# Performance work log

Measured on AMD Instinct MI355X. Metric: run time of the kernel, lower is better.

## Reference

```python
import jax, jax.numpy as jnp
import numpy as np

H, C, PQ, PV = 12, 16, 4, 8  # heads, scalar head dim, query points, value points
EPS = 1e-8


def setup_inputs() -> dict:
    key = jax.random.key(0)
    ks = jax.random.split(key, 16)
    B, N, S, Z = 2, 512, 384, 128
    def w(k, fan_in, shape):
        return jax.random.normal(k, shape, jnp.float32) / np.sqrt(fan_in)
    return {
        's': jax.random.normal(ks[0], (B, N, S), jnp.float32),
        'z': jax.random.normal(ks[1], (B, N, N, Z), jnp.float32),
        'R': jax.random.normal(ks[2], (B, N, 3, 3), jnp.float32),
        't': jax.random.normal(ks[3], (B, N, 3), jnp.float32),
        'Wq': w(ks[4], S, (S, H * C)),
        'Wk': w(ks[5], S, (S, H * C)),
        'Wv': w(ks[6], S, (S, H * C)),
        'Wqp': w(ks[7], S, (S, H * PQ * 3)),
        'Wkp': w(ks[8], S, (S, H * PQ * 3)),
        'Wvp': w(ks[9], S, (S, H * PV * 3)),
        'Wb': w(ks[10], Z, (Z, H)),
        'head_weights': jax.random.normal(ks[11], (H,), jnp.float32) * 0.1,
        'Wout': w(ks[12], H * (C + 4 * PV + Z), (H * (C + 4 * PV + Z), S)),
    }


def reference(s, z, R, t, Wq, Wk, Wv, Wqp, Wkp, Wvp, Wb, head_weights, Wout):
    B, N, _ = s.shape
    Zc = z.shape[-1]
    # scalar q/k/v: [B,N,H,C]
    q = (s @ Wq).reshape(B, N, H, C)
    k = (s @ Wk).reshape(B, N, H, C)
    v = (s @ Wv).reshape(B, N, H, C)
    # point q/k/v in local frames, then map to global: x_g = R x + t
    def to_global(Wp, P):
        p = (s @ Wp).reshape(B, N, H, P, 3)
        return jnp.einsum('bnxy,bnhpy->bnhpx', R, p) + t[:, :, None, None, :]
    qp = to_global(Wqp, PQ)   # [B,N,H,PQ,3]
    kp = to_global(Wkp, PQ)
    vp = to_global(Wvp, PV)   # [B,N,H,PV,3]
    # pair bias [B,H,N,N]
    b = jnp.einsum('bijz,zh->bhij', z, Wb)
    # scalar attention logits
    scal = jnp.einsum('bihc,bjhc->bhij', q, k) / np.sqrt(C)
    # squared point distances via expansion (avoid [B,N,N,H,PQ,3] tensor)
    qq = jnp.sum(qp * qp, axis=(-1, -2))                    # [B,N,H]
    kk = jnp.sum(kp * kp, axis=(-1, -2))                    # [B,N,H]
    qk = jnp.einsum('bihpx,bjhpx->bhij', qp, kp)
    dist2 = qq.transpose(0, 2, 1)[:, :, :, None] + kk.transpose(0, 2, 1)[:, :, None, :] - 2.0 * qk
    gamma = jax.nn.softplus(head_weights)                   # [H]
    wC = np.sqrt(2.0 / (9.0 * PQ))
    wL = np.sqrt(1.0 / 3.0)
    logits = wL * (scal + b) - (wL * wC / 2.0) * gamma[None, :, None, None] * dist2
    a = jax.nn.softmax(logits, axis=-1)                     # [B,H,N,N]
    # scalar output
    o = jnp.einsum('bhij,bjhc->bihc', a, v).reshape(B, N, H * C)
    # point output: aggregate in global frame, then back to local: R^T (x - t)
    opt_g = jnp.einsum('bhij,bjhpx->bihpx', a, vp)
    d = opt_g - t[:, :, None, None, :]
    opt = jnp.einsum('bnyx,bnhpy->bnhpx', R, d)             # R^T d
    opt_norm = jnp.sqrt(jnp.sum(opt * opt, axis=-1) + EPS)  # [B,N,H,PV]
    # pair output
    opair = jnp.einsum('bhij,bijz->bihz', a, z).reshape(B, N, H * Zc)
    cat = jnp.concatenate([o, opt.reshape(B, N, H * PV * 3),
                           opt_norm.reshape(B, N, H * PV), opair], axis=-1)
    return cat @ Wout
```

## Files before the change

kernel.cpp:

```cpp
#include <hip/hip_runtime.h>
#include <math.h>

#define BB 2
#define NN 512
#define SDIM 384
#define ZDIM 128
#define HH 12
#define CDIM 16
#define PQ 4
#define PV 8
#define BN (BB*NN)
#define CATD 2112

#define WL  0.57735026918962576f
#define LAM 0.06804138174397717f

#define OFF_Q    0
#define OFF_QP   196608
#define OFF_QQ   344064
#define OFF_KT4  356352
#define OFF_KPT4 552960
#define OFF_KKT  700416
#define OFF_V    712704
#define OFF_VP   909312
#define OFF_BIAS 1204224
#define OFF_CAT  7495680

__device__ __forceinline__ float dot4(float4 a, float4 b) {
    return a.x*b.x + a.y*b.y + a.z*b.z + a.w*b.w;
}
__device__ __forceinline__ void fma4(float4& a, float s, float4 b) {
    a.x += s*b.x; a.y += s*b.y; a.z += s*b.z; a.w += s*b.w;
}
__device__ __forceinline__ void add4(float4& a, float4 b) {
    a.x += b.x; a.y += b.y; a.z += b.z; a.w += b.w;
}
__device__ __forceinline__ void mul4(float4& a, float s) {
    a.x *= s; a.y *= s; a.z *= s; a.w *= s;
}

__global__ __launch_bounds__(256) void k_proj(
    const float* __restrict__ s, const float* __restrict__ Rg, const float* __restrict__ tg,
    const float* __restrict__ Wq, const float* __restrict__ Wk, const float* __restrict__ Wv,
    const float* __restrict__ Wqp, const float* __restrict__ Wkp, const float* __restrict__ Wvp,
    float* __restrict__ ws)
{
    __shared__ float4 pL4[2][144];
    __shared__ float  sqL[2][96];
    __shared__ float  Rt[2][12];
    const int t = threadIdx.x;
    const int n0 = blockIdx.x * 2;
    const int b  = n0 >> 9;
    const int nloc = n0 & 511;

    if (t < 24) {
        int rr = t / 12, c = t % 12;
        Rt[rr][c] = (c < 9) ? Rg[(n0+rr)*9 + c] : tg[(n0+rr)*3 + (c-9)];
    }
    const float* s0 = s + (size_t)n0*SDIM;
    const float* s1 = s0 + SDIM;
    __syncthreads();

    float4* Q4g  = (float4*)(ws + OFF_Q);
    float4* V4g  = (float4*)(ws + OFF_V);
    float4* KT4g = (float4*)(ws + OFF_KT4);

    for (int it = 0; it < 2; ++it) {
        int g = t + it*256;
        if (g >= 288) break;
        const float4* W4; int wc4, ld4, dst;
        if (g < 48)       { W4 = (const float4*)Wq;  wc4 = g;     ld4 = 48; dst = 0; }
        else if (g < 96)  { W4 = (const float4*)Wk;  wc4 = g-48;  ld4 = 48; dst = 1; }
        else if (g < 144) { W4 = (const float4*)Wv;  wc4 = g-96;  ld4 = 48; dst = 2; }
        else if (g < 180) { W4 = (const float4*)Wqp; wc4 = g-144; ld4 = 36; dst = 3; }
        else if (g < 216) { W4 = (const float4*)Wkp; wc4 = g-180; ld4 = 36; dst = 4; }
        else              { W4 = (const float4*)Wvp; wc4 = g-216; ld4 = 72; dst = 5; }
        float4 acc0 = {0,0,0,0}, acc1 = {0,0,0,0};
        #pragma unroll 4
        for (int r = 0; r < SDIM; ++r) {
            float4 wv = W4[r*ld4 + wc4];
            float f0 = s0[r], f1 = s1[r];
            fma4(acc0, f0, wv);
            fma4(acc1, f1, wv);
        }
        if (dst == 0) {
            Q4g[(size_t)n0*48 + wc4] = acc0;
            Q4g[(size_t)(n0+1)*48 + wc4] = acc1;
        } else if (dst == 1) {
            size_t base = ((size_t)(b*48 + wc4))*512 + nloc;
            KT4g[base] = acc0; KT4g[base+1] = acc1;
        } else if (dst == 2) {
            V4g[(size_t)n0*48 + wc4] = acc0;
            V4g[(size_t)(n0+1)*48 + wc4] = acc1;
        } else if (dst == 3) {
            pL4[0][wc4] = acc0; pL4[1][wc4] = acc1;
        } else if (dst == 4) {
            pL4[0][36+wc4] = acc0; pL4[1][36+wc4] = acc1;
        } else {
            pL4[0][72+wc4] = acc0; pL4[1][72+wc4] = acc1;
        }
    }
    __syncthreads();

    for (int task = t; task < 384; task += 256) {
        int rr = task / 192, pt = task % 192;
        const float* pl = (const float*)pL4[rr];
        int off = (pt < 48) ? pt*3 : (pt < 96 ? 144 + (pt-48)*3 : 288 + (pt-96)*3);
        float p0 = pl[off], p1 = pl[off+1], p2 = pl[off+2];
        const float* R = Rt[rr];
        float g0 = R[0]*p0 + R[1]*p1 + R[2]*p2 + R[9];
        float g1 = R[3]*p0 + R[4]*p1 + R[5]*p2 + R[10];
        float g2 = R[6]*p0 + R[7]*p1 + R[8]*p2 + R[11];
        int bn = n0 + rr, n = bn & 511;
        if (pt < 48) {
            int o = pt*3;
            float* d = ws + OFF_QP + (size_t)bn*144 + o;
            d[0] = g0; d[1] = g1; d[2] = g2;
            sqL[rr][pt] = g0*g0 + g1*g1 + g2*g2;
        } else if (pt < 96) {
            int pc = (pt-48)*3;
            float gg[3] = {g0,g1,g2};
            #pragma unroll
            for (int x = 0; x < 3; ++x) {
                int pcx = pc + x;
                ws[OFF_KPT4 + (((size_t)(b*36 + (pcx>>2)))*512 + n)*4 + (pcx&3)] = gg[x];
            }
            sqL[rr][pt] = g0*g0 + g1*g1 + g2*g2;
        } else {
            int o = (pt-96)*3;
            float* d = ws + OFF_VP + (size_t)bn*288 + o;
            d[0] = g0; d[1] = g1; d[2] = g2;
        }
    }
    __syncthreads();

    if (t < 48) {
        int rr = t / 24, u = t % 24;
        int bn = n0 + rr, n = bn & 511;
        if (u < 12) {
            float sm = sqL[rr][u*4] + sqL[rr][u*4+1] + sqL[rr][u*4+2] + sqL[rr][u*4+3];
            ws[OFF_QQ + (size_t)bn*12 + u] = sm;
        } else {
            int h = u - 12;
            float sm = sqL[rr][48+h*4] + sqL[rr][48+h*4+1] + sqL[rr][48+h*4+2] + sqL[rr][48+h*4+3];
            ws[OFF_KKT + ((size_t)(b*12 + h))*512 + n] = sm;
        }
    }
}

__global__ __launch_bounds__(256) void k_bias(
    const float* __restrict__ z, const float* __restrict__ Wb, float* __restrict__ ws)
{
    __shared__ __align__(16) float4 zsh[64*33];
    const int t = threadIdx.x;
    const int blk = blockIdx.x;
    const int bi = blk >> 3;
    const int j0 = (blk & 7) * 64;
    const float4* zg = (const float4*)z + ((size_t)bi*512 + j0)*32;
    #pragma unroll
    for (int k = 0; k < 8; ++k) {
        const int i = t + 256*k;
        zsh[(i>>5)*33 + (i&31)] = zg[i];
    }
    __syncthreads();

    const int j  = t >> 2;
    const int hg = t & 3;
    float a0 = 0.f, a1 = 0.f, a2 = 0.f;
    const float4* row = &zsh[j*33];
    #pragma unroll 8
    for (int c4 = 0; c4 < 32; ++c4) {
        const float4 zq = row[c4];
        const float* wb = Wb + c4*48;
        #pragma unroll
        for (int e = 0; e < 4; ++e) {
            const float zv = ((const float*)&zq)[e];
            const float* w = wb + e*12;
            a0 += zv * w[hg];
            a1 += zv * w[hg+4];
            a2 += zv * w[hg+8];
        }
    }
    float* BI = ws + OFF_BIAS + (size_t)bi*HH*512 + j0 + j;
    BI[(hg  )*512] = a0;
    BI[(hg+4)*512] = a1;
    BI[(hg+8)*512] = a2;
}

__global__ __launch_bounds__(512, 2) void k_attn(
    const float* __restrict__ z, const float* __restrict__ Rg, const float* __restrict__ tg,
    const float* __restrict__ hw, float* __restrict__ ws)
{
    __shared__ __align__(16) float aL[HH*516];
    __shared__ float4 optgS4[72];
    __shared__ float RiL[9], tiL[3], sInv[12];

    const int t = threadIdx.x;
    const int d = blockIdx.x;
    const int xcd = d & 7, slot = d >> 3;
    const int bi = (xcd < 4) ? (xcd*128 + slot) : (512 + (xcd-4)*128 + slot);
    const int b = bi >> 9;

    if (t < 9)             RiL[t]   = Rg[bi*9 + t];
    if (t >= 9 && t < 12)  tiL[t-9] = tg[bi*3 + (t-9)];

    float gam[HH];
    #pragma unroll
    for (int h = 0; h < HH; ++h) {
        float x = hw[h];
        gam[h] = (x > 20.f) ? x : log1pf(__expf(x));
    }

    {
        const int j = t;
        const float4* Q4u  = (const float4*)(ws + OFF_Q  + (size_t)bi*192);
        const float4* QP4u = (const float4*)(ws + OFF_QP + (size_t)bi*144);
        const float*  QQu  = ws + OFF_QQ + (size_t)bi*12;
        const float4* KT4  = (const float4*)(ws + OFF_KT4)  + (size_t)b*48*512;
        const float4* KPT4 = (const float4*)(ws + OFF_KPT4) + (size_t)b*36*512;
        const float*  KKT  = ws + OFF_KKT  + (size_t)b*12*512;
        const float*  BI   = ws + OFF_BIAS + (size_t)bi*HH*512;
        for (int h = 0; h < HH; ++h) {
            float scal = 0.f, qk = 0.f;
            #pragma unroll
            for (int cg = 0; cg < 4; ++cg)
                scal += dot4(Q4u[h*4+cg], KT4[(h*4+cg)*512 + j]);
            #pragma unroll
            for (int pg = 0; pg < 3; ++pg)
                qk += dot4(QP4u[h*3+pg], KPT4[(h*3+pg)*512 + j]);
            float dist2 = QQu[h] + KKT[h*512 + j] - 2.f*qk;
            aL[h*516 + j] = WL*(scal*0.25f + BI[h*512 + j]) - LAM*gam[h]*dist2;
        }
    }
    __syncthreads();

    {
        const int w = t >> 6, lane = t & 63;
        for (int h = w; h < HH; h += 8) {
            float* row = aL + h*516;
            float m = -1e30f;
            #pragma unroll
            for (int k = 0; k < 8; ++k) m = fmaxf(m, row[lane + 64*k]);
            #pragma unroll
            for (int off = 32; off > 0; off >>= 1) m = fmaxf(m, __shfl_xor(m, off));
            float ssum = 0.f;
            #pragma unroll
            for (int k = 0; k < 8; ++k) {
                float e = __expf(row[lane + 64*k] - m);
                row[lane + 64*k] = e;
                ssum += e;
            }
            #pragma unroll
            for (int off = 32; off > 0; off >>= 1) ssum += __shfl_xor(ssum, off);
            if (lane == 0) sInv[h] = 1.f / ssum;
        }
    }
    __syncthreads();

    float4 acc0 = {0,0,0,0}, acc1 = {0,0,0,0}, acc2 = {0,0,0,0};
    int rid = -1, seg = 0;

#define FMA8(ZB, AP0, AP1, AP2, JT) do { \
    float4 av0 = *(const float4*)((AP0) + (JT)); \
    float4 av1 = *(const float4*)((AP1) + (JT)); \
    float4 av2 = *(const float4*)((AP2) + (JT)); \
    float4 aw0 = *(const float4*)((AP0) + (JT) + 4); \
    float4 aw1 = *(const float4*)((AP1) + (JT) + 4); \
    float4 aw2 = *(const float4*)((AP2) + (JT) + 4); \
    fma4(acc0, av0.x, ZB[0]); fma4(acc1, av1.x, ZB[0]); fma4(acc2, av2.x, ZB[0]); \
    fma4(acc0, av0.y, ZB[1]); fma4(acc1, av1.y, ZB[1]); fma4(acc2, av2.y, ZB[1]); \
    fma4(acc0, av0.z, ZB[2]); fma4(acc1, av1.z, ZB[2]); fma4(acc2, av2.z, ZB[2]); \
    fma4(acc0, av0.w, ZB[3]); fma4(acc1, av1.w, ZB[3]); fma4(acc2, av2.w, ZB[3]); \
    fma4(acc0, aw0.x, ZB[4]); fma4(acc1, aw1.x, ZB[4]); fma4(acc2, aw2.x, ZB[4]); \
    fma4(acc0, aw0.y, ZB[5]); fma4(acc1, aw1.y, ZB[5]); fma4(acc2, aw2.y, ZB[5]); \
    fma4(acc0, aw0.z, ZB[6]); fma4(acc1, aw1.z, ZB[6]); fma4(acc2, aw2.z, ZB[6]); \
    fma4(acc0, aw0.w, ZB[7]); fma4(acc1, aw1.w, ZB[7]); fma4(acc2, aw2.w, ZB[7]); \
} while (0)

    if (t < 384) {
        seg = t >> 7;
        rid = t & 127;
        const int hg = rid >> 5, zc4 = rid & 31;
        const int j0 = seg*176;
        const int ngrp = (seg == 2) ? 20 : 22;
        const float4* Zp = (const float4*)z + (size_t)bi*512*32 + zc4;
        const float* a0p = aL + hg*516;
        const float* a1p = aL + (hg+4)*516;
        const float* a2p = aL + (hg+8)*516;
        float4 zA[8], zB[8];
        #pragma unroll
        for (int e = 0; e < 8; ++e) zA[e] = Zp[(size_t)(j0+e)*32];
        for (int p = 0; p < ngrp; p += 2) {
            const int jt = j0 + p*8;
            #pragma unroll
            for (int e = 0; e < 8; ++e) zB[e] = Zp[(size_t)(jt+8+e)*32];
            FMA8(zA, a0p, a1p, a2p, jt);
            if (p + 2 < ngrp) {
                #pragma unroll
                for (int e = 0; e < 8; ++e) zA[e] = Zp[(size_t)(jt+16+e)*32];
            }
            FMA8(zB, a0p, a1p, a2p, jt + 8);
        }
    } else if (t < 504) {
        const int v = t - 384;
        seg = v / 40;
        const int w = v % 40;
        rid = 128 + w;
        const int j0 = seg*176, j1 = (seg == 2) ? 512 : j0 + 176;
        const float4* P; int S, D, O, hg;
        if (w < 16) {
            hg = w >> 2; S = 48; D = 16; O = hg*4 + (w & 3);
            P = (const float4*)(ws + OFF_V) + (size_t)b*512*48;
        } else {
            const int v2 = w - 16;
            hg = v2 / 6; S = 72; D = 24; O = hg*6 + v2 % 6;
            P = (const float4*)(ws + OFF_VP) + (size_t)b*512*72;
        }
        const float* a0p = aL + hg*516;
        const float* a1p = aL + (hg+4)*516;
        const float* a2p = aL + (hg+8)*516;
        #pragma unroll 2
        for (int jt = j0; jt < j1; jt += 4) {
            float4 av0 = *(const float4*)(a0p + jt);
            float4 av1 = *(const float4*)(a1p + jt);
            float4 av2 = *(const float4*)(a2p + jt);
            #pragma unroll
            for (int e = 0; e < 4; ++e) {
                const size_t base = (size_t)(jt+e)*S + O;
                fma4(acc0, ((const float*)&av0)[e], P[base]);
                fma4(acc1, ((const float*)&av1)[e], P[base + D]);
                fma4(acc2, ((const float*)&av2)[e], P[base + 2*D]);
            }
        }
    }
    __syncthreads();
    float4* sc4 = (float4*)aL;
    if (rid >= 0) {
        const int si = (seg*168 + rid)*3;
        sc4[si] = acc0; sc4[si+1] = acc1; sc4[si+2] = acc2;
    }
    __syncthreads();

    if (t < 168) {
        float4 r0 = {0,0,0,0}, r1 = {0,0,0,0}, r2 = {0,0,0,0};
        #pragma unroll
        for (int ss = 0; ss < 3; ++ss) {
            const int si = (ss*168 + t)*3;
            add4(r0, sc4[si]); add4(r1, sc4[si+1]); add4(r2, sc4[si+2]);
        }
        int typ, hg;
        if (t < 128)      { typ = 0; hg = t >> 5; }
        else if (t < 144) { typ = 1; hg = (t-128) >> 2; }
        else              { typ = 2; hg = (t-144) / 6; }
        mul4(r0, sInv[hg]); mul4(r1, sInv[hg+4]); mul4(r2, sInv[hg+8]);
        float4* cat4 = (float4*)(ws + OFF_CAT);
        const size_t cb = (size_t)bi * 528;
        if (typ == 0) {
            const int zc4 = t & 31;
            cat4[cb + 144 + (hg  )*32 + zc4] = r0;
            cat4[cb + 144 + (hg+4)*32 + zc4] = r1;
            cat4[cb + 144 + (hg+8)*32 + zc4] = r2;
        } else if (typ == 1) {
            const int c4 = (t-128) & 3;
            cat4[cb + (hg  )*4 + c4] = r0;
            cat4[cb + (hg+4)*4 + c4] = r1;
            cat4[cb + (hg+8)*4 + c4] = r2;
        } else {
            const int po = (t-144) % 6;
            optgS4[(hg  )*6 + po] = r0;
            optgS4[(hg+4)*6 + po] = r1;
            optgS4[(hg+8)*6 + po] = r2;
        }
    }
    __syncthreads();

    if (t < 96) {
        const float* og = (const float*)optgS4;
        int h = t >> 3, p = t & 7;
        int o = h*24 + p*3;
        float d0 = og[o]   - tiL[0];
        float d1 = og[o+1] - tiL[1];
        float d2 = og[o+2] - tiL[2];
        float ox = RiL[0]*d0 + RiL[3]*d1 + RiL[6]*d2;
        float oy = RiL[1]*d0 + RiL[4]*d1 + RiL[7]*d2;
        float oz = RiL[2]*d0 + RiL[5]*d1 + RiL[8]*d2;
        float* cat = ws + OFF_CAT + (size_t)bi*CATD;
        cat[192 + o]     = ox;
        cat[192 + o + 1] = oy;
        cat[192 + o + 2] = oz;
        cat[480 + h*8 + p] = sqrtf(ox*ox + oy*oy + oz*oz + 1e-8f);
    }
}

__global__ __launch_bounds__(384) void k_out(
    const float* __restrict__ Wout, const float* __restrict__ ws, float* __restrict__ out)
{
    const int t = threadIdx.x;
    const int row0 = blockIdx.x * 4;
    const float* c0 = ws + OFF_CAT + (size_t)(row0+0)*CATD;
    const float* c1 = c0 + CATD;
    const float* c2 = c1 + CATD;
    const float* c3 = c2 + CATD;
    float a0 = 0.f, a1 = 0.f, a2 = 0.f, a3 = 0.f;
    #pragma unroll 8
    for (int r = 0; r < CATD; ++r) {
        float w = Wout[(size_t)r*384 + t];
        a0 += c0[r]*w; a1 += c1[r]*w; a2 += c2[r]*w; a3 += c3[r]*w;
    }
    out[(size_t)(row0+0)*384 + t] = a0;
    out[(size_t)(row0+1)*384 + t] = a1;
    out[(size_t)(row0+2)*384 + t] = a2;
    out[(size_t)(row0+3)*384 + t] = a3;
}

extern "C" void kernel_launch(void* const* d_in, const int* in_sizes, int n_in,
                              void* d_out, int out_size, void* d_ws, size_t ws_size,
                              hipStream_t stream)
{
    const float* s    = (const float*)d_in[0];
    const float* z    = (const float*)d_in[1];
    const float* R    = (const float*)d_in[2];
    const float* tt   = (const float*)d_in[3];
    const float* Wq   = (const float*)d_in[4];
    const float* Wk   = (const float*)d_in[5];
    const float* Wv   = (const float*)d_in[6];
    const float* Wqp  = (const float*)d_in[7];
    const float* Wkp  = (const float*)d_in[8];
    const float* Wvp  = (const float*)d_in[9];
    const float* Wb   = (const float*)d_in[10];
    const float* hw   = (const float*)d_in[11];
    const float* Wout = (const float*)d_in[12];
    float* ws  = (float*)d_ws;
    float* out = (float*)d_out;

    hipLaunchKernelGGL(k_proj, dim3(BN/2),     dim3(256), 0, stream,
                       s, R, tt, Wq, Wk, Wv, Wqp, Wkp, Wvp, ws);
    hipLaunchKernelGGL(k_bias, dim3(BN*NN/64), dim3(256), 0, stream, z, Wb, ws);
    hipLaunchKernelGGL(k_attn, dim3(BN),       dim3(512), 0, stream, z, R, tt, hw, ws);
    hipLaunchKernelGGL(k_out,  dim3(BN/4),     dim3(384), 0, stream, Wout, ws, out);
}
```

Before: 803.3 us.

## Fuse pair-bias projection into attention kernel, drop separate bias pass

Removes the standalone k_bias kernel and computes the z·Wb pair bias per (i,j) directly inside k_attn, with each thread reading its own z row from global memory. This avoids writing and re-reading the bias buffer and saves one launch. z still has to be read again later for the pair-output aggregation. The in-kernel reads are strided per thread (each thread reads a 512-byte row), and the 12 extra accumulators add register pressure under launch_bounds(512,2).

```diff
diff --git a/kernel.cpp b/kernel.cpp
--- a/kernel.cpp
+++ b/kernel.cpp
@@ -23,7 +23,6 @@
 #define OFF_KKT  700416
 #define OFF_V    712704
 #define OFF_VP   909312
-#define OFF_BIAS 1204224
 #define OFF_CAT  7495680
 
 __device__ __forceinline__ float dot4(float4 a, float4 b) {
@@ -148,48 +147,9 @@
     }
 }
 
-__global__ __launch_bounds__(256) void k_bias(
-    const float* __restrict__ z, const float* __restrict__ Wb, float* __restrict__ ws)
-{
-    __shared__ __align__(16) float4 zsh[64*33];
-    const int t = threadIdx.x;
-    const int blk = blockIdx.x;
-    const int bi = blk >> 3;
-    const int j0 = (blk & 7) * 64;
-    const float4* zg = (const float4*)z + ((size_t)bi*512 + j0)*32;
-    #pragma unroll
-    for (int k = 0; k < 8; ++k) {
-        const int i = t + 256*k;
-        zsh[(i>>5)*33 + (i&31)] = zg[i];
-    }
-    __syncthreads();
-
-    const int j  = t >> 2;
-    const int hg = t & 3;
-    float a0 = 0.f, a1 = 0.f, a2 = 0.f;
-    const float4* row = &zsh[j*33];
-    #pragma unroll 8
-    for (int c4 = 0; c4 < 32; ++c4) {
-        const float4 zq = row[c4];
-        const float* wb = Wb + c4*48;
-        #pragma unroll
-        for (int e = 0; e < 4; ++e) {
-            const float zv = ((const float*)&zq)[e];
-            const float* w = wb + e*12;
-            a0 += zv * w[hg];
-            a1 += zv * w[hg+4];
-            a2 += zv * w[hg+8];
-        }
-    }
-    float* BI = ws + OFF_BIAS + (size_t)bi*HH*512 + j0 + j;
-    BI[(hg  )*512] = a0;
-    BI[(hg+4)*512] = a1;
-    BI[(hg+8)*512] = a2;
-}
-
 __global__ __launch_bounds__(512, 2) void k_attn(
     const float* __restrict__ z, const float* __restrict__ Rg, const float* __restrict__ tg,
-    const float* __restrict__ hw, float* __restrict__ ws)
+    const float* __restrict__ hw, const float* __restrict__ Wb, float* __restrict__ ws)
 {
     __shared__ __align__(16) float aL[HH*516];
     __shared__ float4 optgS4[72];
@@ -213,13 +173,28 @@
 
     {
         const int j = t;
+        float pb[HH];
+        #pragma unroll
+        for (int h = 0; h < HH; ++h) pb[h] = 0.f;
+        const float4* zrow4 = (const float4*)z + ((size_t)bi*512 + j)*32;
+        #pragma unroll 4
+        for (int c4 = 0; c4 < 32; ++c4) {
+            const float4 zq = zrow4[c4];
+            const float* wb = Wb + c4*48;
+            #pragma unroll
+            for (int e = 0; e < 4; ++e) {
+                const float zv = ((const float*)&zq)[e];
+                const float* w = wb + e*12;
+                #pragma unroll
+                for (int h = 0; h < HH; ++h) pb[h] += zv * w[h];
+            }
+        }
         const float4* Q4u  = (const float4*)(ws + OFF_Q  + (size_t)bi*192);
         const float4* QP4u = (const float4*)(ws + OFF_QP + (size_t)bi*144);
         const float*  QQu  = ws + OFF_QQ + (size_t)bi*12;
         const float4* KT4  = (const float4*)(ws + OFF_KT4)  + (size_t)b*48*512;
         const float4* KPT4 = (const float4*)(ws + OFF_KPT4) + (size_t)b*36*512;
         const float*  KKT  = ws + OFF_KKT  + (size_t)b*12*512;
-        const float*  BI   = ws + OFF_BIAS + (size_t)bi*HH*512;
         for (int h = 0; h < HH; ++h) {
             float scal = 0.f, qk = 0.f;
             #pragma unroll
@@ -229,7 +204,7 @@
             for (int pg = 0; pg < 3; ++pg)
                 qk += dot4(QP4u[h*3+pg], KPT4[(h*3+pg)*512 + j]);
             float dist2 = QQu[h] + KKT[h*512 + j] - 2.f*qk;
-            aL[h*516 + j] = WL*(scal*0.25f + BI[h*512 + j]) - LAM*gam[h]*dist2;
+            aL[h*516 + j] = WL*(scal*0.25f + pb[h]) - LAM*gam[h]*dist2;
         }
     }
     __syncthreads();
@@ -433,9 +408,8 @@
     float* ws  = (float*)d_ws;
     float* out = (float*)d_out;
 
-    hipLaunchKernelGGL(k_proj, dim3(BN/2),     dim3(256), 0, stream,
+    hipLaunchKernelGGL(k_proj, dim3(BN/2), dim3(256), 0, stream,
                        s, R, tt, Wq, Wk, Wv, Wqp, Wkp, Wvp, ws);
-    hipLaunchKernelGGL(k_bias, dim3(BN*NN/64), dim3(256), 0, stream, z, Wb, ws);
-    hipLaunchKernelGGL(k_attn, dim3(BN),       dim3(512), 0, stream, z, R, tt, hw, ws);
-    hipLaunchKernelGGL(k_out,  dim3(BN/4),     dim3(384), 0, stream, Wout, ws, out);
-}
+    hipLaunchKernelGGL(k_attn, dim3(BN),   dim3(512), 0, stream, z, R, tt, hw, Wb, ws);
+    hipLaunchKernelGGL(k_out,  dim3(BN/4), dim3(384), 0, stream, Wout, ws, out);
+}
```

Measured after the change: 739.9 us. 7.9% less time.
